# Kernel optimization log

Measured on AMD Instinct MI355X. Metric: run time of the kernel, lower is better.

## Reference

```python
import jax, jax.numpy as jnp
from jax import lax
import numpy as np

B, F_BINS, T_TOTAL = 32, 128, 2400
H = 256           # cell_size
SEG = 24          # segment_size
S = T_TOTAL // SEG  # num_segments (T divisible by SEG)
SCALE = 1.0 / np.sqrt(H)


def _lstm_params(key, in_dim, hid_dim):
    k1, k2, k3, k4 = jax.random.split(key, 4)
    return (jax.random.normal(k1, (4 * hid_dim, in_dim), jnp.float32) * SCALE,
            jax.random.normal(k2, (4 * hid_dim, hid_dim), jnp.float32) * SCALE,
            jax.random.normal(k3, (4 * hid_dim,), jnp.float32) * SCALE,
            jax.random.normal(k4, (4 * hid_dim,), jnp.float32) * SCALE)


def setup_inputs() -> dict:
    key = jax.random.key(0)
    ks = jax.random.split(key, 5)
    inp = jax.random.normal(ks[0], (B, F_BINS, T_TOTAL), jnp.float32)
    oe = _lstm_params(ks[1], F_BINS, H)   # outer_encoder
    ie = _lstm_params(ks[2], H, H)        # inner_encoder
    idp = _lstm_params(ks[3], H, H)       # inner_decoder
    od = _lstm_params(ks[4], H, F_BINS)   # outer_decoder (hidden = input_size)
    d = {"inp": inp}
    for name, p in (("oe", oe), ("ie", ie), ("id", idp), ("od", od)):
        d[f"{name}_wih"], d[f"{name}_whh"], d[f"{name}_bih"], d[f"{name}_bhh"] = p
    return d


def run_lstm(x, w_ih, w_hh, b_ih, b_hh):
    """torch nn.LSTM (1 layer, batch_first). x: (N, T, I) -> outputs (N,T,Hd), h_T, c_T."""
    N = x.shape[0]
    Hd = w_hh.shape[1]
    # precompute input contribution for all steps: (N, T, 4H)
    xw = jnp.einsum('nti,gi->ntg', x, w_ih) + b_ih + b_hh

    def step(carry, xg):
        h, c = carry
        g = xg + h @ w_hh.T              # (N, 4H), gate order i,f,g,o
        i, f, gg, o = jnp.split(g, 4, axis=-1)
        c = jax.nn.sigmoid(f) * c + jax.nn.sigmoid(i) * jnp.tanh(gg)
        h = jax.nn.sigmoid(o) * jnp.tanh(c)
        return (h, c), h

    h0 = jnp.zeros((N, Hd), x.dtype)
    (hT, cT), ys = lax.scan(step, (h0, h0), jnp.swapaxes(xw, 0, 1))
    return jnp.swapaxes(ys, 0, 1), hT, cT


def reference(inp, oe_wih, oe_whh, oe_bih, oe_bhh,
              ie_wih, ie_whh, ie_bih, ie_bhh,
              id_wih, id_whh, id_bih, id_bhh,
              od_wih, od_whh, od_bih, od_bhh):
    x = jnp.swapaxes(inp, 1, 2)                      # (B, T, F)
    # outer encoder: all segments batched (independent in the original loop)
    segs = x.reshape(B * S, SEG, F_BINS)
    _, _, c_seg = run_lstm(segs, oe_wih, oe_whh, oe_bih, oe_bhh)   # (B*S, H)
    cell_state_tensor = c_seg.reshape(B, S, H)
    # inner encoder over segment cell-states -> bottleneck cell
    _, _, bottleneck = run_lstm(cell_state_tensor, ie_wih, ie_whh, ie_bih, ie_bhh)  # (B, H)
    # inner decoder: bottleneck repeated num_segments times
    dec_in = jnp.broadcast_to(bottleneck[:, None, :], (B, S, H))
    dec_out, _, _ = run_lstm(dec_in, id_wih, id_whh, id_bih, id_bhh)  # (B, S, H)
    # outer decoder: each segment code repeated SEG steps, batched over segments
    od_in = jnp.broadcast_to(dec_out.reshape(B * S, 1, H), (B * S, SEG, H))
    rec, _, _ = run_lstm(od_in, od_wih, od_whh, od_bih, od_bhh)       # (B*S, SEG, F)
    rec = rec.reshape(B, T_TOTAL, F_BINS)
    return jnp.swapaxes(rec, 1, 2)                   # (B, F, T)
```

## Files before the change

kernel.cpp:

```cpp
#include <hip/hip_runtime.h>


#define B_    32
#define F_    128
#define T_    2400
#define H_    256
#define SEG_  24
#define S_    100
#define NSEQ_ 3200

using v2h = __attribute__((ext_vector_type(2))) _Float16;
using v4h = __attribute__((ext_vector_type(4))) _Float16;
using v8h = __attribute__((ext_vector_type(8))) _Float16;
using v4f = __attribute__((ext_vector_type(4))) float;

#ifndef __has_builtin
#define __has_builtin(x) 0
#endif

__device__ __forceinline__ float fdot2f(v2h a, v2h b, float c) {
#if __has_builtin(__builtin_amdgcn_fdot2)
  return __builtin_amdgcn_fdot2(a, b, c, false);
#else
  return c + (float)a[0] * (float)b[0] + (float)a[1] * (float)b[1];
#endif
}

__device__ __forceinline__ v2h ext8(v8h v, int e) {
  v2h r; r[0] = v[2 * e]; r[1] = v[2 * e + 1]; return r;
}
__device__ __forceinline__ v2h ext4(v4h v, int e) {
  v2h r; r[0] = v[2 * e]; r[1] = v[2 * e + 1]; return r;
}

__device__ __forceinline__ float sigm(float x) { return 1.f / (1.f + __expf(-x)); }
__device__ __forceinline__ float tanh_f(float x) { return 1.f - 2.f / (__expf(2.f * x) + 1.f); }

__global__ void k_wt2(v2h* __restrict__ dst, const float* __restrict__ w1, int K1,
                      const float* __restrict__ w2, int K2src, int G, int n) {
  int idx = blockIdx.x * 256 + threadIdx.x;
  if (idx >= n) return;
  int k2 = idx / G, g = idx - k2 * G;
  int k = 2 * k2;
  float v0, v1;
  if (k < K1) {
    v0 = w1[(size_t)g * K1 + k];
    v1 = w1[(size_t)g * K1 + k + 1];
  } else {
    int kk = k - K1;
    v0 = w2[(size_t)g * K2src + kk];
    v1 = w2[(size_t)g * K2src + kk + 1];
  }
  v2h r;
  r[0] = (_Float16)v0;
  r[1] = (_Float16)v1;
  dst[idx] = r;
}

__global__ void k_f16(_Float16* __restrict__ dst, const float* __restrict__ src, int n) {
  int i = blockIdx.x * 256 + threadIdx.x;
  if (i < n) dst[i] = (_Float16)src[i];
}

__global__ void k_wpack_oe(v8h* __restrict__ dst, const float* __restrict__ wih,
                           const float* __restrict__ whh) {
  int idx = blockIdx.x * 256 + threadIdx.x;
  if (idx >= 12 * 64 * 64) return;
  int lane = idx & 63;
  int nt = (idx >> 6) & 63;
  int kc = idx >> 12;
  int col = nt * 16 + (lane & 15);
  int k0 = kc * 32 + (lane >> 4) * 8;
  v8h r;
#pragma unroll
  for (int j = 0; j < 8; ++j) {
    int k = k0 + j;
    float v = (k < 128) ? wih[(size_t)col * 128 + k] : whh[(size_t)col * 256 + (k - 128)];
    r[j] = (_Float16)v;
  }
  dst[idx] = r;
}

__global__ void k_wpack_od(v8h* __restrict__ dst, const float* __restrict__ whh) {
  int idx = blockIdx.x * 256 + threadIdx.x;
  if (idx >= 4 * 32 * 64) return;
  int lane = idx & 63;
  int nt = (idx >> 6) & 31;
  int kc = idx >> 11;
  int col = nt * 16 + (lane & 15);
  int k0 = kc * 32 + (lane >> 4) * 8;
  v8h r;
#pragma unroll
  for (int j = 0; j < 8; ++j) r[j] = (_Float16)whh[(size_t)col * 128 + k0 + j];
  dst[idx] = r;
}

__global__ void k_tin(const float* __restrict__ inp, _Float16* __restrict__ xT) {
  __shared__ float tile[32][33];
  int b = blockIdx.z, f0 = blockIdx.y * 32, t0 = blockIdx.x * 32;
  int tx = threadIdx.x, ty = threadIdx.y;
#pragma unroll
  for (int r = 0; r < 4; ++r) {
    int f = f0 + ty + 8 * r;
    tile[ty + 8 * r][tx] = inp[((size_t)b * F_ + f) * T_ + t0 + tx];
  }
  __syncthreads();
#pragma unroll
  for (int r = 0; r < 4; ++r) {
    int tau = t0 + ty + 8 * r;
    xT[((size_t)b * T_ + tau) * F_ + f0 + tx] = (_Float16)tile[tx][ty + 8 * r];
  }
}

__global__ void k_tout(const float* __restrict__ rec, float* __restrict__ out) {
  __shared__ float tile[32][33];
  int b = blockIdx.z, f0 = blockIdx.y * 32, t0 = blockIdx.x * 32;
  int tx = threadIdx.x, ty = threadIdx.y;
#pragma unroll
  for (int r = 0; r < 4; ++r) {
    int tau = t0 + ty + 8 * r;
    tile[ty + 8 * r][tx] = rec[((size_t)b * T_ + tau) * F_ + f0 + tx];
  }
  __syncthreads();
#pragma unroll
  for (int r = 0; r < 4; ++r) {
    int f = f0 + ty + 8 * r;
    out[((size_t)b * F_ + f) * T_ + t0 + tx] = tile[tx][ty + 8 * r];
  }
}

__global__ __launch_bounds__(512, 2) void k_outer_enc_mfma(
    const v8h* __restrict__ wpack,
    const _Float16* __restrict__ xT,
    const float* __restrict__ bih, const float* __restrict__ bhh,
    float* __restrict__ cst) {
  __shared__ __align__(16) _Float16 a2[32][392];
  const int tid = threadIdx.x;
  const int w = tid >> 6;
  const int lane = tid & 63;
  const int cI = lane & 15;
  const int q = lane >> 4;
  const int seq0 = blockIdx.x * 32;

  float bias[4][2];
#pragma unroll
  for (int g = 0; g < 4; ++g)
#pragma unroll
    for (int jt = 0; jt < 2; ++jt) {
      int col = g * 256 + w * 32 + jt * 16 + cI;
      bias[g][jt] = bih[col] + bhh[col];
    }

  for (int i = tid; i < 32 * 256; i += 512) a2[i >> 8][128 + (i & 255)] = (_Float16)0.f;
  {
    int row = tid >> 4, ch = tid & 15;
    v8h xv = ((const v8h*)(xT + ((size_t)(seq0 + row) * SEG_ + 0) * F_))[ch];
    *(v8h*)(&a2[row][ch * 8]) = xv;
  }
  __syncthreads();

  float cs[2][2][4];
#pragma unroll
  for (int mt = 0; mt < 2; ++mt)
#pragma unroll
    for (int jt = 0; jt < 2; ++jt)
#pragma unroll
      for (int r = 0; r < 4; ++r) cs[mt][jt][r] = 0.f;

  for (int t = 0; t < SEG_; ++t) {
    v4f C[2][8];
#pragma unroll
    for (int mt = 0; mt < 2; ++mt)
#pragma unroll
      for (int n = 0; n < 8; ++n) {
        v4f z = {0.f, 0.f, 0.f, 0.f};
        C[mt][n] = z;
      }
    v8h Bf[2][8];
#pragma unroll
    for (int n = 0; n < 8; ++n) {
      int nt = (n >> 1) * 16 + w * 2 + (n & 1);
      Bf[0][n] = wpack[(size_t)(0 * 64 + nt) * 64 + lane];
    }
#pragma unroll 2
    for (int kc = 0; kc < 12; ++kc) {
      int cur = kc & 1, nxt = cur ^ 1;
      if (kc < 11) {
#pragma unroll
        for (int n = 0; n < 8; ++n) {
          int nt = (n >> 1) * 16 + w * 2 + (n & 1);
          Bf[nxt][n] = wpack[(size_t)((kc + 1) * 64 + nt) * 64 + lane];
        }
      }
      v8h A0 = *(const v8h*)(&a2[0 * 16 + cI][kc * 32 + q * 8]);
      v8h A1 = *(const v8h*)(&a2[1 * 16 + cI][kc * 32 + q * 8]);
#pragma unroll
      for (int n = 0; n < 8; ++n) {
        C[0][n] = __builtin_amdgcn_mfma_f32_16x16x32_f16(A0, Bf[cur][n], C[0][n], 0, 0, 0);
        C[1][n] = __builtin_amdgcn_mfma_f32_16x16x32_f16(A1, Bf[cur][n], C[1][n], 0, 0, 0);
      }
    }
    __syncthreads();
#pragma unroll
    for (int mt = 0; mt < 2; ++mt)
#pragma unroll
      for (int jt = 0; jt < 2; ++jt)
#pragma unroll
        for (int r = 0; r < 4; ++r) {
          float gi = sigm(C[mt][0 * 2 + jt][r] + bias[0][jt]);
          float gf = sigm(C[mt][1 * 2 + jt][r] + bias[1][jt]);
          float gg = tanh_f(C[mt][2 * 2 + jt][r] + bias[2][jt]);
          float go = sigm(C[mt][3 * 2 + jt][r] + bias[3][jt]);
          float cc = gf * cs[mt][jt][r] + gi * gg;
          cs[mt][jt][r] = cc;
          float h = go * tanh_f(cc);
          a2[mt * 16 + q * 4 + r][128 + w * 32 + jt * 16 + cI] = (_Float16)h;
        }
    if (t < SEG_ - 1) {
      int row = tid >> 4, ch = tid & 15;
      v8h xv = ((const v8h*)(xT + ((size_t)(seq0 + row) * SEG_ + (t + 1)) * F_))[ch];
      *(v8h*)(&a2[row][ch * 8]) = xv;
    }
    __syncthreads();
  }
#pragma unroll
  for (int mt = 0; mt < 2; ++mt)
#pragma unroll
    for (int jt = 0; jt < 2; ++jt)
#pragma unroll
      for (int r = 0; r < 4; ++r)
        cst[(size_t)(seq0 + mt * 16 + q * 4 + r) * H_ + w * 32 + jt * 16 + cI] = cs[mt][jt][r];
}

__global__ __launch_bounds__(512, 2) void k_outer_dec_mfma(
    const v8h* __restrict__ wpack,
    const float* __restrict__ xw,
    float* __restrict__ rec) {
  __shared__ __align__(16) _Float16 ah[32][136];
  const int tid = threadIdx.x;
  const int w = tid >> 6;
  const int lane = tid & 63;
  const int cI = lane & 15;
  const int q = lane >> 4;
  const int seq0 = blockIdx.x * 32;

  v8h Bf[4][4];
#pragma unroll
  for (int kc = 0; kc < 4; ++kc)
#pragma unroll
    for (int g = 0; g < 4; ++g)
      Bf[kc][g] = wpack[(size_t)(kc * 32 + g * 8 + w) * 64 + lane];

  float xwr[2][4][4];
#pragma unroll
  for (int mt = 0; mt < 2; ++mt)
#pragma unroll
    for (int r = 0; r < 4; ++r) {
      int row = seq0 + mt * 16 + q * 4 + r;
#pragma unroll
      for (int g = 0; g < 4; ++g)
        xwr[mt][r][g] = xw[(size_t)row * 512 + g * 128 + w * 16 + cI];
    }

  for (int i = tid; i < 32 * 128; i += 512) ah[i >> 7][i & 127] = (_Float16)0.f;
  __syncthreads();

  float cs[2][4];
#pragma unroll
  for (int mt = 0; mt < 2; ++mt)
#pragma unroll
    for (int r = 0; r < 4; ++r) cs[mt][r] = 0.f;

  for (int t = 0; t < SEG_; ++t) {
    v4f C[2][4];
#pragma unroll
    for (int mt = 0; mt < 2; ++mt)
#pragma unroll
      for (int g = 0; g < 4; ++g) {
        v4f z = {0.f, 0.f, 0.f, 0.f};
        C[mt][g] = z;
      }
#pragma unroll
    for (int kc = 0; kc < 4; ++kc) {
      v8h A0 = *(const v8h*)(&ah[0 * 16 + cI][kc * 32 + q * 8]);
      v8h A1 = *(const v8h*)(&ah[1 * 16 + cI][kc * 32 + q * 8]);
#pragma unroll
      for (int g = 0; g < 4; ++g) {
        C[0][g] = __builtin_amdgcn_mfma_f32_16x16x32_f16(A0, Bf[kc][g], C[0][g], 0, 0, 0);
        C[1][g] = __builtin_amdgcn_mfma_f32_16x16x32_f16(A1, Bf[kc][g], C[1][g], 0, 0, 0);
      }
    }
    __syncthreads();
#pragma unroll
    for (int mt = 0; mt < 2; ++mt)
#pragma unroll
      for (int r = 0; r < 4; ++r) {
        float gi = sigm(C[mt][0][r] + xwr[mt][r][0]);
        float gf = sigm(C[mt][1][r] + xwr[mt][r][1]);
        float gg = tanh_f(C[mt][2][r] + xwr[mt][r][2]);
        float go = sigm(C[mt][3][r] + xwr[mt][r][3]);
        float cc = gf * cs[mt][r] + gi * gg;
        cs[mt][r] = cc;
        float h = go * tanh_f(cc);
        int row = mt * 16 + q * 4 + r;
        ah[row][w * 16 + cI] = (_Float16)h;
        rec[((size_t)(seq0 + row) * SEG_ + t) * 128 + w * 16 + cI] = h;
      }
    __syncthreads();
  }
}

template <int GT>
__global__ __launch_bounds__(256) void k_proj(
    const float* __restrict__ A, const v2h* __restrict__ wt2,
    const float* __restrict__ b1, const float* __restrict__ b2,
    float* __restrict__ out) {
  constexpr int G = GT * 256;
  __shared__ __align__(16) _Float16 a2[16][256];
  const int tid = threadIdx.x;
  const size_t row0 = (size_t)blockIdx.x * 16;
  for (int idx = tid; idx < 16 * 256; idx += 256) {
    int r = idx >> 8, k = idx & 255;
    a2[r][k] = (_Float16)A[(row0 + (size_t)r) * 256 + k];
  }
  __syncthreads();
  float acc[16][GT];
#pragma unroll
  for (int r = 0; r < 16; ++r)
#pragma unroll
    for (int q = 0; q < GT; ++q) acc[r][q] = 0.f;
  const v2h* wp = wt2 + tid;
#pragma unroll 2
  for (int k2 = 0; k2 < 128; ++k2) {
    v2h w[GT];
#pragma unroll
    for (int q = 0; q < GT; ++q) w[q] = wp[256 * q];
    wp += G;
#pragma unroll
    for (int r = 0; r < 16; ++r) {
      v2h a = ((const v2h*)&a2[r][0])[k2];
#pragma unroll
      for (int q = 0; q < GT; ++q) acc[r][q] = fdot2f(w[q], a, acc[r][q]);
    }
  }
#pragma unroll
  for (int q = 0; q < GT; ++q) {
    float bias = b1[tid + 256 * q] + b2[tid + 256 * q];
#pragma unroll
    for (int r = 0; r < 16; ++r)
      out[(row0 + (size_t)r) * G + tid + 256 * q] = acc[r][q] + bias;
  }
}

__global__ __launch_bounds__(512) void k_inner(
    const _Float16* __restrict__ whh,
    const float* __restrict__ xw, long xw_seq_stride, long xw_t_stride, int T,
    float* __restrict__ h_out,
    float* __restrict__ c_out) {
  __shared__ __align__(16) _Float16 ah[H_];
  __shared__ __align__(16) _Float16 wo[H_][260];
  const int t_ = threadIdx.x;
  const int p = t_ >> 1;
  const int hf = t_ & 1;
  const int b = blockIdx.x;

  v8h wv[3][16];
#pragma unroll
  for (int r = 0; r < 3; ++r) {
    const v8h* src = (const v8h*)(whh + ((size_t)(H_ * r + p)) * H_ + hf * 128);
#pragma unroll
    for (int q = 0; q < 16; ++q) wv[r][q] = src[q];
  }
  {
    const v4h* src = (const v4h*)(whh + ((size_t)(H_ * 3 + p)) * H_ + hf * 128);
    v4h* dst = (v4h*)&wo[p][hf * 128];
#pragma unroll
    for (int q = 0; q < 32; ++q) dst[q] = src[q];
  }
  if (t_ < H_) ah[t_] = (_Float16)0.f;
  float c = 0.f;
  __syncthreads();

  for (int t = 0; t < T; ++t) {
    const float* xwp = xw + (size_t)b * xw_seq_stride + (size_t)t * xw_t_stride;
    float x0 = xwp[p], x1 = xwp[H_ + p], x2 = xwp[2 * H_ + p], x3 = xwp[3 * H_ + p];
    float a0 = 0.f, a1 = 0.f, a2 = 0.f, a3 = 0.f;
    const v8h* A8 = ((const v8h*)ah) + hf * 16;
    const v4h* O4 = (const v4h*)&wo[p][hf * 128];
#pragma unroll
    for (int q = 0; q < 16; ++q) {
      v8h av = A8[q];
      v8h w0v = wv[0][q], w1v = wv[1][q], w2v = wv[2][q];
      v4h o0 = O4[2 * q], o1 = O4[2 * q + 1];
#pragma unroll
      for (int e = 0; e < 4; ++e) {
        v2h ap = ext8(av, e);
        a0 = fdot2f(ext8(w0v, e), ap, a0);
        a1 = fdot2f(ext8(w1v, e), ap, a1);
        a2 = fdot2f(ext8(w2v, e), ap, a2);
        v2h op = (e < 2) ? ext4(o0, e) : ext4(o1, e - 2);
        a3 = fdot2f(op, ap, a3);
      }
    }
    a0 += __shfl_xor(a0, 1);
    a1 += __shfl_xor(a1, 1);
    a2 += __shfl_xor(a2, 1);
    a3 += __shfl_xor(a3, 1);
    float gi = sigm(a0 + x0);
    float gf = sigm(a1 + x1);
    float gg = tanh_f(a2 + x2);
    float go = sigm(a3 + x3);
    c = gf * c + gi * gg;
    float h = go * tanh_f(c);
    __syncthreads();
    if (hf == 0) {
      ah[p] = (_Float16)h;
      if (h_out) h_out[((size_t)b * T + t) * H_ + p] = h;
    }
    __syncthreads();
  }
  if (c_out && hf == 0) c_out[(size_t)b * H_ + p] = c;
}

extern "C" void kernel_launch(void* const* d_in, const int* in_sizes, int n_in,
                              void* d_out, int out_size, void* d_ws, size_t ws_size,
                              hipStream_t stream) {
  const float* inp    = (const float*)d_in[0];
  const float* oe_wih = (const float*)d_in[1];
  const float* oe_whh = (const float*)d_in[2];
  const float* oe_bih = (const float*)d_in[3];
  const float* oe_bhh = (const float*)d_in[4];
  const float* ie_wih = (const float*)d_in[5];
  const float* ie_whh = (const float*)d_in[6];
  const float* ie_bih = (const float*)d_in[7];
  const float* ie_bhh = (const float*)d_in[8];
  const float* id_wih = (const float*)d_in[9];
  const float* id_whh = (const float*)d_in[10];
  const float* id_bih = (const float*)d_in[11];
  const float* id_bhh = (const float*)d_in[12];
  const float* od_wih = (const float*)d_in[13];
  const float* od_whh = (const float*)d_in[14];
  const float* od_bih = (const float*)d_in[15];
  const float* od_bhh = (const float*)d_in[16];

  char* ws = (char*)d_ws;
  _Float16* xT     = (_Float16*)(ws + 0);
  v8h* wpack_oe    = (v8h*)(ws + 19660800);
  float* cst       = (float*)(ws + 20447232);
  v2h* wt2_ie      = (v2h*)(ws + 23724032);
  float* xw_ie     = (float*)(ws + 24248320);
  _Float16* whh_ie = (_Float16*)(ws + 37355520);
  float* bott      = (float*)(ws + 37879808);
  v2h* wt2_id      = (v2h*)(ws + 37912576);
  float* xw_id     = (float*)(ws + 38436864);
  _Float16* whh_id = (_Float16*)(ws + 38567936);
  float* dec       = (float*)(ws + 39092224);
  v2h* wt2_odih    = (v2h*)(ws + 42369024);
  float* xw_od     = (float*)(ws + 42631168);
  v8h* wpack_od    = (v8h*)(ws + 49184768);
  float* rec       = (float*)(ws + 49315840);

  k_wpack_oe<<<dim3(192), dim3(256), 0, stream>>>(wpack_oe, oe_wih, oe_whh);
  k_wt2<<<dim3(512), dim3(256), 0, stream>>>(wt2_ie, ie_wih, 256, nullptr, 0, 1024, 128 * 1024);
  k_wt2<<<dim3(512), dim3(256), 0, stream>>>(wt2_id, id_wih, 256, nullptr, 0, 1024, 128 * 1024);
  k_wt2<<<dim3(256), dim3(256), 0, stream>>>(wt2_odih, od_wih, 256, nullptr, 0, 512, 128 * 512);
  k_wpack_od<<<dim3(32), dim3(256), 0, stream>>>(wpack_od, od_whh);
  k_f16<<<dim3(1024), dim3(256), 0, stream>>>(whh_ie, ie_whh, 262144);
  k_f16<<<dim3(1024), dim3(256), 0, stream>>>(whh_id, id_whh, 262144);

  k_tin<<<dim3(75, 4, 32), dim3(32, 8), 0, stream>>>(inp, xT);
  k_outer_enc_mfma<<<dim3(100), dim3(512), 0, stream>>>(wpack_oe, xT, oe_bih, oe_bhh, cst);
  k_proj<4><<<dim3(200), dim3(256), 0, stream>>>(cst, wt2_ie, ie_bih, ie_bhh, xw_ie);
  k_inner<<<dim3(32), dim3(512), 0, stream>>>(whh_ie, xw_ie, (long)S_ * 1024, 1024, S_, nullptr, bott);
  k_proj<4><<<dim3(2), dim3(256), 0, stream>>>(bott, wt2_id, id_bih, id_bhh, xw_id);
  k_inner<<<dim3(32), dim3(512), 0, stream>>>(whh_id, xw_id, 1024, 0, S_, dec, nullptr);
  k_proj<2><<<dim3(200), dim3(256), 0, stream>>>(dec, wt2_odih, od_bih, od_bhh, xw_od);
  k_outer_dec_mfma<<<dim3(100), dim3(512), 0, stream>>>(wpack_od, xw_od, rec);
  k_tout<<<dim3(75, 4, 32), dim3(32, 8), 0, stream>>>(rec, (float*)d_out);

  (void)in_sizes; (void)n_in; (void)out_size; (void)ws_size;
}
```

Before: 990.5 us.

## Cache first weight chunks in LDS, reorder weight pack, use raw barriers

The outer-encoder weight pack is reordered so each wave's tiles are contiguous. The first two K-chunks are staged once into shared memory, and the remaining chunks stream from global through a rotating register double-buffer that prefetches the next timestep's first chunks. The next-step input load is issued at the top of each step, and __syncthreads is replaced by raw s_barrier macros that skip the vmcnt wait, which is meant to cut barrier stalls in all recurrent kernels. This raises LDS use and register pressure, and it depends on the hand-written waitcnt placement being correct.

```diff
diff --git a/kernel.cpp b/kernel.cpp
--- a/kernel.cpp
+++ b/kernel.cpp
@@ -17,6 +17,20 @@
 #ifndef __has_builtin
 #define __has_builtin(x) 0
 #endif
+
+#define BARRIER_RAW()                                  \
+  do {                                                 \
+    __builtin_amdgcn_sched_barrier(0);                 \
+    asm volatile("s_barrier" ::: "memory");            \
+    __builtin_amdgcn_sched_barrier(0);                 \
+  } while (0)
+
+#define BARRIER_LGKM()                                            \
+  do {                                                            \
+    __builtin_amdgcn_sched_barrier(0);                            \
+    asm volatile("s_waitcnt lgkmcnt(0)\n\ts_barrier" ::: "memory"); \
+    __builtin_amdgcn_sched_barrier(0);                            \
+  } while (0)
 
 __device__ __forceinline__ float fdot2f(v2h a, v2h b, float c) {
 #if __has_builtin(__builtin_amdgcn_fdot2)
@@ -65,10 +79,12 @@
 __global__ void k_wpack_oe(v8h* __restrict__ dst, const float* __restrict__ wih,
                            const float* __restrict__ whh) {
   int idx = blockIdx.x * 256 + threadIdx.x;
-  if (idx >= 12 * 64 * 64) return;
+  if (idx >= 12 * 8 * 8 * 64) return;
   int lane = idx & 63;
-  int nt = (idx >> 6) & 63;
+  int n = (idx >> 6) & 7;
+  int wv = (idx >> 9) & 7;
   int kc = idx >> 12;
+  int nt = (n >> 1) * 16 + wv * 2 + (n & 1);
   int col = nt * 16 + (lane & 15);
   int k0 = kc * 32 + (lane >> 4) * 8;
   v8h r;
@@ -135,6 +151,7 @@
     const float* __restrict__ bih, const float* __restrict__ bhh,
     float* __restrict__ cst) {
   __shared__ __align__(16) _Float16 a2[32][392];
+  __shared__ __align__(16) v8h wc[2 * 8 * 8 * 64];
   const int tid = threadIdx.x;
   const int w = tid >> 6;
   const int lane = tid & 63;
@@ -151,6 +168,12 @@
       bias[g][jt] = bih[col] + bhh[col];
     }
 
+  {
+    const int4* src = (const int4*)wpack;
+    int4* dst = (int4*)wc;
+    for (int i = tid; i < 2 * 8 * 8 * 64; i += 512) dst[i] = src[i];
+  }
+
   for (int i = tid; i < 32 * 256; i += 512) a2[i >> 8][128 + (i & 255)] = (_Float16)0.f;
   {
     int row = tid >> 4, ch = tid & 15;
@@ -159,6 +182,13 @@
   }
   __syncthreads();
 
+  v8h Bf[2][8];
+#pragma unroll
+  for (int n = 0; n < 8; ++n) {
+    Bf[0][n] = wpack[((size_t)(2 * 8 + w) * 8 + n) * 64 + lane];
+    Bf[1][n] = wpack[((size_t)(3 * 8 + w) * 8 + n) * 64 + lane];
+  }
+
   float cs[2][2][4];
 #pragma unroll
   for (int mt = 0; mt < 2; ++mt)
@@ -167,7 +197,12 @@
 #pragma unroll
       for (int r = 0; r < 4; ++r) cs[mt][jt][r] = 0.f;
 
+#pragma unroll 1
   for (int t = 0; t < SEG_; ++t) {
+    const int xrow = tid >> 4, xch = tid & 15;
+    const int tnext = (t < SEG_ - 1) ? t + 1 : t;
+    v8h xv = ((const v8h*)(xT + ((size_t)(seq0 + xrow) * SEG_ + tnext) * F_))[xch];
+
     v4f C[2][8];
 #pragma unroll
     for (int mt = 0; mt < 2; ++mt)
@@ -176,31 +211,37 @@
         v4f z = {0.f, 0.f, 0.f, 0.f};
         C[mt][n] = z;
       }
-    v8h Bf[2][8];
-#pragma unroll
-    for (int n = 0; n < 8; ++n) {
-      int nt = (n >> 1) * 16 + w * 2 + (n & 1);
-      Bf[0][n] = wpack[(size_t)(0 * 64 + nt) * 64 + lane];
-    }
-#pragma unroll 2
-    for (int kc = 0; kc < 12; ++kc) {
-      int cur = kc & 1, nxt = cur ^ 1;
-      if (kc < 11) {
-#pragma unroll
-        for (int n = 0; n < 8; ++n) {
-          int nt = (n >> 1) * 16 + w * 2 + (n & 1);
-          Bf[nxt][n] = wpack[(size_t)((kc + 1) * 64 + nt) * 64 + lane];
-        }
-      }
-      v8h A0 = *(const v8h*)(&a2[0 * 16 + cI][kc * 32 + q * 8]);
-      v8h A1 = *(const v8h*)(&a2[1 * 16 + cI][kc * 32 + q * 8]);
+
+#pragma unroll
+    for (int c = 0; c < 2; ++c) {
+      v8h A0 = *(const v8h*)(&a2[0 * 16 + cI][c * 32 + q * 8]);
+      v8h A1 = *(const v8h*)(&a2[1 * 16 + cI][c * 32 + q * 8]);
 #pragma unroll
       for (int n = 0; n < 8; ++n) {
-        C[0][n] = __builtin_amdgcn_mfma_f32_16x16x32_f16(A0, Bf[cur][n], C[0][n], 0, 0, 0);
-        C[1][n] = __builtin_amdgcn_mfma_f32_16x16x32_f16(A1, Bf[cur][n], C[1][n], 0, 0, 0);
-      }
-    }
-    __syncthreads();
+        v8h Bc = wc[((c * 8 + w) * 8 + n) * 64 + lane];
+        C[0][n] = __builtin_amdgcn_mfma_f32_16x16x32_f16(A0, Bc, C[0][n], 0, 0, 0);
+        C[1][n] = __builtin_amdgcn_mfma_f32_16x16x32_f16(A1, Bc, C[1][n], 0, 0, 0);
+      }
+    }
+
+#pragma unroll
+    for (int i = 2; i <= 11; ++i) {
+      const int s = i & 1;
+      v8h A0 = *(const v8h*)(&a2[0 * 16 + cI][i * 32 + q * 8]);
+      v8h A1 = *(const v8h*)(&a2[1 * 16 + cI][i * 32 + q * 8]);
+#pragma unroll
+      for (int n = 0; n < 8; ++n) {
+        C[0][n] = __builtin_amdgcn_mfma_f32_16x16x32_f16(A0, Bf[s][n], C[0][n], 0, 0, 0);
+        C[1][n] = __builtin_amdgcn_mfma_f32_16x16x32_f16(A1, Bf[s][n], C[1][n], 0, 0, 0);
+      }
+      const int p = (i <= 9) ? (i + 2) : (i - 8);
+#pragma unroll
+      for (int n = 0; n < 8; ++n)
+        Bf[s][n] = wpack[((size_t)(p * 8 + w) * 8 + n) * 64 + lane];
+    }
+
+    BARRIER_RAW();
+
 #pragma unroll
     for (int mt = 0; mt < 2; ++mt)
 #pragma unroll
@@ -216,13 +257,11 @@
           float h = go * tanh_f(cc);
           a2[mt * 16 + q * 4 + r][128 + w * 32 + jt * 16 + cI] = (_Float16)h;
         }
-    if (t < SEG_ - 1) {
-      int row = tid >> 4, ch = tid & 15;
-      v8h xv = ((const v8h*)(xT + ((size_t)(seq0 + row) * SEG_ + (t + 1)) * F_))[ch];
-      *(v8h*)(&a2[row][ch * 8]) = xv;
-    }
-    __syncthreads();
-  }
+    *(v8h*)(&a2[xrow][xch * 8]) = xv;
+
+    BARRIER_LGKM();
+  }
+
 #pragma unroll
   for (int mt = 0; mt < 2; ++mt)
 #pragma unroll
@@ -271,6 +310,7 @@
 #pragma unroll
     for (int r = 0; r < 4; ++r) cs[mt][r] = 0.f;
 
+#pragma unroll 1
   for (int t = 0; t < SEG_; ++t) {
     v4f C[2][4];
 #pragma unroll
@@ -290,7 +330,7 @@
         C[1][g] = __builtin_amdgcn_mfma_f32_16x16x32_f16(A1, Bf[kc][g], C[1][g], 0, 0, 0);
       }
     }
-    __syncthreads();
+    BARRIER_RAW();
 #pragma unroll
     for (int mt = 0; mt < 2; ++mt)
 #pragma unroll
@@ -306,7 +346,7 @@
         ah[row][w * 16 + cI] = (_Float16)h;
         rec[((size_t)(seq0 + row) * SEG_ + t) * 128 + w * 16 + cI] = h;
       }
-    __syncthreads();
+    BARRIER_LGKM();
   }
 }
 
@@ -381,6 +421,7 @@
   float c = 0.f;
   __syncthreads();
 
+#pragma unroll 1
   for (int t = 0; t < T; ++t) {
     const float* xwp = xw + (size_t)b * xw_seq_stride + (size_t)t * xw_t_stride;
     float x0 = xwp[p], x1 = xwp[H_ + p], x2 = xwp[2 * H_ + p], x3 = xwp[3 * H_ + p];
@@ -412,12 +453,12 @@
     float go = sigm(a3 + x3);
     c = gf * c + gi * gg;
     float h = go * tanh_f(c);
-    __syncthreads();
+    BARRIER_RAW();
     if (hf == 0) {
       ah[p] = (_Float16)h;
       if (h_out) h_out[((size_t)b * T + t) * H_ + p] = h;
     }
-    __syncthreads();
+    BARRIER_LGKM();
   }
   if (c_out && hf == 0) c_out[(size_t)b * H_ + p] = c;
 }
```

Result: slower. 1.236 ms (+24.8%).

## Stream outer-encoder weight chunks into LDS via async global_load_lds double buffering

Applied to the files above, without the earlier changes.

The outer encoder MFMA kernel used to read weight fragments straight from global memory into registers on every K chunk. It now copies each 64KB weight chunk into a double-buffered LDS area with global_load_lds DMA and reads the B fragments from LDS, with a barrier per K chunk. The 128KB LDS buffer forces occupancy down to one block per CU (launch bounds changed to 512,1). Several time loops are also marked unroll 1. The aim is to overlap weight fetch with MFMA work and cut register pressure, at the cost of extra syncs and lower occupancy.

```diff
diff --git a/kernel.cpp b/kernel.cpp
--- a/kernel.cpp
+++ b/kernel.cpp
@@ -17,6 +17,12 @@
 #ifndef __has_builtin
 #define __has_builtin(x) 0
 #endif
+
+__device__ __forceinline__ void dma16(const void* g, void* l) {
+  __builtin_amdgcn_global_load_lds(
+      (const __attribute__((address_space(1))) void*)g,
+      (__attribute__((address_space(3))) void*)l, 16, 0, 0);
+}
 
 __device__ __forceinline__ float fdot2f(v2h a, v2h b, float c) {
 #if __has_builtin(__builtin_amdgcn_fdot2)
@@ -129,12 +135,13 @@
   }
 }
 
-__global__ __launch_bounds__(512, 2) void k_outer_enc_mfma(
+__global__ __launch_bounds__(512, 1) void k_outer_enc_mfma(
     const v8h* __restrict__ wpack,
     const _Float16* __restrict__ xT,
     const float* __restrict__ bih, const float* __restrict__ bhh,
     float* __restrict__ cst) {
   __shared__ __align__(16) _Float16 a2[32][392];
+  __shared__ __align__(16) v8h wbuf[2 * 4096];
   const int tid = threadIdx.x;
   const int w = tid >> 6;
   const int lane = tid & 63;
@@ -157,6 +164,12 @@
     v8h xv = ((const v8h*)(xT + ((size_t)(seq0 + row) * SEG_ + 0) * F_))[ch];
     *(v8h*)(&a2[row][ch * 8]) = xv;
   }
+  {
+    const char* gs = (const char*)wpack + tid * 16;
+    char* ls = (char*)wbuf + (tid >> 6) * 1024;
+#pragma unroll
+    for (int i = 0; i < 8; ++i) dma16(gs + i * 8192, ls + i * 8192);
+  }
   __syncthreads();
 
   float cs[2][2][4];
@@ -167,6 +180,7 @@
 #pragma unroll
       for (int r = 0; r < 4; ++r) cs[mt][jt][r] = 0.f;
 
+#pragma unroll 1
   for (int t = 0; t < SEG_; ++t) {
     v4f C[2][8];
 #pragma unroll
@@ -176,31 +190,32 @@
         v4f z = {0.f, 0.f, 0.f, 0.f};
         C[mt][n] = z;
       }
-    v8h Bf[2][8];
-#pragma unroll
-    for (int n = 0; n < 8; ++n) {
-      int nt = (n >> 1) * 16 + w * 2 + (n & 1);
-      Bf[0][n] = wpack[(size_t)(0 * 64 + nt) * 64 + lane];
-    }
-#pragma unroll 2
+
+#pragma unroll
     for (int kc = 0; kc < 12; ++kc) {
-      int cur = kc & 1, nxt = cur ^ 1;
-      if (kc < 11) {
-#pragma unroll
-        for (int n = 0; n < 8; ++n) {
-          int nt = (n >> 1) * 16 + w * 2 + (n & 1);
-          Bf[nxt][n] = wpack[(size_t)((kc + 1) * 64 + nt) * 64 + lane];
-        }
-      }
+      if (kc) __syncthreads();
+
+      {
+        const int nc = (kc + 1) % 12;
+        const char* gs = (const char*)wpack + (size_t)nc * 65536 + tid * 16;
+        char* ls = (char*)wbuf + ((kc + 1) & 1) * 65536 + (tid >> 6) * 1024;
+#pragma unroll
+        for (int i = 0; i < 8; ++i) dma16(gs + i * 8192, ls + i * 8192);
+      }
+
+      const v8h* bb = wbuf + (kc & 1) * 4096;
       v8h A0 = *(const v8h*)(&a2[0 * 16 + cI][kc * 32 + q * 8]);
       v8h A1 = *(const v8h*)(&a2[1 * 16 + cI][kc * 32 + q * 8]);
 #pragma unroll
       for (int n = 0; n < 8; ++n) {
-        C[0][n] = __builtin_amdgcn_mfma_f32_16x16x32_f16(A0, Bf[cur][n], C[0][n], 0, 0, 0);
-        C[1][n] = __builtin_amdgcn_mfma_f32_16x16x32_f16(A1, Bf[cur][n], C[1][n], 0, 0, 0);
-      }
-    }
-    __syncthreads();
+        int nt = (n >> 1) * 16 + w * 2 + (n & 1);
+        v8h Bv = bb[nt * 64 + lane];
+        C[0][n] = __builtin_amdgcn_mfma_f32_16x16x32_f16(A0, Bv, C[0][n], 0, 0, 0);
+        C[1][n] = __builtin_amdgcn_mfma_f32_16x16x32_f16(A1, Bv, C[1][n], 0, 0, 0);
+      }
+    }
+    __syncthreads();
+
 #pragma unroll
     for (int mt = 0; mt < 2; ++mt)
 #pragma unroll
@@ -271,6 +286,7 @@
 #pragma unroll
     for (int r = 0; r < 4; ++r) cs[mt][r] = 0.f;
 
+#pragma unroll 1
   for (int t = 0; t < SEG_; ++t) {
     v4f C[2][4];
 #pragma unroll
@@ -381,6 +397,7 @@
   float c = 0.f;
   __syncthreads();
 
+#pragma unroll 1
   for (int t = 0; t < T; ++t) {
     const float* xwp = xw + (size_t)b * xw_seq_stride + (size_t)t * xw_t_stride;
     float x0 = xwp[p], x1 = xwp[H_ + p], x2 = xwp[2 * H_ + p], x3 = xwp[3 * H_ + p];
```

After: 1.215 ms. 1.23x slower.
